# Performance work log

Hardware: AMD Instinct MI355X
Metric: run time of the kernel (lower is better)

The kernel has to match this reference:

```python
import jax, jax.numpy as jnp
import numpy as np

N = 65536
INPUT_DIM = 4
HIDDEN = 256
OUT_DIM = 64
NUM_FREQS = 10
NUM_LAYERS = 4  # -> 3 residual blocks
NUM_COMPOSE = 4
DIN_PE = INPUT_DIM + 2 * INPUT_DIM * NUM_FREQS  # 84


def setup_inputs() -> dict:
    key = jax.random.key(0)
    ks = jax.random.split(key, 10)
    x = jax.random.uniform(ks[0], (N, INPUT_DIM), jnp.float32, 0.1, 1.0)
    in_dim = jax.random.uniform(ks[1], (N,), jnp.float32, 0.5, 1.5)
    layer_id = jax.random.randint(ks[2], (N,), 0, NUM_COMPOSE, dtype=jnp.int32)
    s0 = 1.0 / np.sqrt(DIN_PE)
    sh = 1.0 / np.sqrt(HIDDEN)
    W0 = jax.random.normal(ks[3], (NUM_COMPOSE, DIN_PE, HIDDEN), jnp.float32) * s0
    b0 = jax.random.normal(ks[4], (NUM_COMPOSE, HIDDEN), jnp.float32) * s0
    Wh = jax.random.normal(ks[5], (NUM_COMPOSE, NUM_LAYERS - 1, HIDDEN, HIDDEN), jnp.float32) * sh
    bh = jax.random.normal(ks[6], (NUM_COMPOSE, NUM_LAYERS - 1, HIDDEN), jnp.float32) * sh
    scal = jax.random.normal(ks[7], (NUM_COMPOSE, NUM_LAYERS - 1), jnp.float32) * 0.5
    Wout = jax.random.normal(ks[8], (NUM_COMPOSE, HIDDEN, OUT_DIM), jnp.float32) * sh
    bout = jax.random.normal(ks[9], (NUM_COMPOSE, OUT_DIM), jnp.float32) * sh
    return {"x": x, "in_dim": in_dim, "layer_id": layer_id, "W0": W0, "b0": b0,
            "Wh": Wh, "bh": bh, "scal": scal, "Wout": Wout, "bout": bout}


def _positional_encoding(x):
    # x: [N, D]; out order matches torch: [x, (sin,cos) for each freq i, each dim j]
    freqs = (2.0 ** jnp.arange(NUM_FREQS, dtype=x.dtype)) * np.pi  # [F]
    ang = x[:, None, :] * freqs[None, :, None]                      # [N, F, D]
    sc = jnp.stack([jnp.sin(ang), jnp.cos(ang)], axis=-1)           # [N, F, D, 2]
    return jnp.concatenate([x, sc.reshape(x.shape[0], -1)], axis=1)  # [N, D+2FD]


def reference(x, in_dim, layer_id, W0, b0, Wh, bh, scal, Wout, bout):
    # x[:, :3] = x[:, :3] / x[:, 3:]
    x = jnp.concatenate([x[:, :3] / x[:, 3:4], x[:, 3:]], axis=1)
    xe = _positional_encoding(x)  # [N, 84]

    def one_model(W0c, b0c, Whc, bhc, sc, Woutc, boutc):
        h = jax.nn.relu(xe @ W0c + b0c)           # [N, H]
        for k in range(NUM_LAYERS - 1):
            h = sc[k] * jax.nn.relu(h @ Whc[k] + bhc[k]) + h
        return h @ Woutc + boutc                  # [N, Dout]

    outs = jax.vmap(one_model)(W0, b0, Wh, bh, scal, Wout, bout)  # [C, N, Dout]
    # dispatch/combine: select each row's expert output
    out = jnp.take_along_axis(outs.transpose(1, 0, 2),
                              layer_id[:, None, None], axis=1)[:, 0]  # [N, Dout]
    return out / in_dim[:, None]
```

## Files before the change

### kernel.cpp

```cpp
#include <hip/hip_runtime.h>
#include <hip/hip_bf16.h>
#include <math.h>

#define N_ROWS 65536
#define H 256
#define DOUT 64
#define NC 4
#define NLAYERS_HIDDEN 3
#define DIN_PE 84
#define KPE 96
#define XE_STRIDE 104
#define BM 64
#define FB_STRIDE 68

#define CHUNK 512
#define WT0_PER_E (3 * 16 * CHUNK)
#define WTH_PER_L (8 * 16 * CHUNK)
#define WTOUT_PER_E (8 * 4 * CHUNK)

using bf16 = __hip_bfloat16;
typedef __bf16 bf16x8 __attribute__((ext_vector_type(8)));
typedef float f32x4 __attribute__((ext_vector_type(4)));

__global__ void bucket_kernel(const int* __restrict__ layer_id,
                              int* __restrict__ gcnt, int* __restrict__ idx) {
  __shared__ int lcnt[NC];
  __shared__ int lbase[NC];
  const int tid = threadIdx.x;
  if (tid < NC) lcnt[tid] = 0;
  __syncthreads();
  const int i = blockIdx.x * blockDim.x + tid;
  const int e = layer_id[i];
  const int lp = atomicAdd(&lcnt[e], 1);
  __syncthreads();
  if (tid < NC) lbase[tid] = atomicAdd(&gcnt[tid], lcnt[tid]);
  __syncthreads();
  idx[e * N_ROWS + lbase[e] + lp] = i;
}

__global__ void prep_weights(const float* __restrict__ W0,
                             const float* __restrict__ Wh,
                             const float* __restrict__ Wout,
                             bf16* __restrict__ wt0, bf16* __restrict__ wth,
                             bf16* __restrict__ wtout) {
  const int n0 = NC * WT0_PER_E;
  const int nh = NC * 3 * WTH_PER_L;
  const int no = NC * WTOUT_PER_E;
  const int total = n0 + nh + no;
  for (int i = blockIdx.x * blockDim.x + threadIdx.x; i < total;
       i += gridDim.x * blockDim.x) {
    if (i < n0) {
      int c = i / WT0_PER_E; int r = i % WT0_PER_E;
      int kbi = r / (16 * CHUNK); int r2 = r % (16 * CHUNK);
      int nblk = r2 / CHUNK; int w = r2 % CHUNK;
      int lane = w / 8, j = w % 8;
      int n = nblk * 16 + (lane & 15);
      int k = kbi * 32 + (lane >> 4) * 8 + j;
      float v = (k < DIN_PE) ? W0[(c * DIN_PE + k) * H + n] : 0.f;
      wt0[i] = __float2bfloat16(v);
    } else if (i < n0 + nh) {
      int u = i - n0;
      int cl = u / WTH_PER_L; int r = u % WTH_PER_L;
      int kbi = r / (16 * CHUNK); int r2 = r % (16 * CHUNK);
      int nblk = r2 / CHUNK; int w = r2 % CHUNK;
      int lane = w / 8, j = w % 8;
      int n = nblk * 16 + (lane & 15);
      int k = kbi * 32 + (lane >> 4) * 8 + j;
      wth[u] = __float2bfloat16(Wh[(cl * H + k) * H + n]);
    } else {
      int u = i - n0 - nh;
      int c = u / WTOUT_PER_E; int r = u % WTOUT_PER_E;
      int kbi = r / (4 * CHUNK); int r2 = r % (4 * CHUNK);
      int nblk = r2 / CHUNK; int w = r2 % CHUNK;
      int lane = w / 8, j = w % 8;
      int n = nblk * 16 + (lane & 15);
      int k = kbi * 32 + (lane >> 4) * 8 + j;
      wtout[u] = __float2bfloat16(Wout[(c * H + k) * DOUT + n]);
    }
  }
}

__global__ __launch_bounds__(256, 3) void mlp_kernel(
    const float* __restrict__ x, const float* __restrict__ in_dim,
    const int* __restrict__ gcnt, const int* __restrict__ idx,
    const bf16* __restrict__ wt0, const float* __restrict__ b0,
    const bf16* __restrict__ wth, const float* __restrict__ bh,
    const float* __restrict__ scal, const bf16* __restrict__ wtout,
    const float* __restrict__ bout, float* __restrict__ out) {
  const int e = blockIdx.y;
  const int cnt = gcnt[e];
  const int base = blockIdx.x * BM;
  if (base >= cnt) return;

  __shared__ int ridx[BM];
  __shared__ float indim_s[BM];
  __shared__ __align__(16) char smem[BM * H * 2];
  bf16* xe = (bf16*)smem;
  bf16* hbuf = (bf16*)smem;
  float* fbuf = (float*)smem;

  const int tid = threadIdx.x;
  if (tid < BM) {
    int p = base + tid;
    int ri = (p < cnt) ? idx[e * N_ROWS + p] : -1;
    ridx[tid] = ri;
    indim_s[tid] = (ri >= 0) ? in_dim[ri] : 1.f;
  }
  __syncthreads();

  {
    const int r = tid >> 2, d = tid & 3;
    const int ri = ridx[r];
    float xd = 0.f, x3 = 1.f;
    if (ri >= 0) { xd = x[ri * 4 + d]; x3 = x[ri * 4 + 3]; }
    float v = (d < 3) ? (xd / x3) : x3;
    if (ri < 0) v = 0.f;
    bf16* row = xe + r * XE_STRIDE;
    row[d] = __float2bfloat16(v);
    float f = 3.14159265358979323846f;
#pragma unroll 1
    for (int q = 0; q < 10; ++q) {
      float sn, cs;
      __sincosf(v * f, &sn, &cs);
      row[4 + q * 8 + d * 2] = __float2bfloat16(sn);
      row[4 + q * 8 + d * 2 + 1] = __float2bfloat16(cs);
      f *= 2.f;
    }
#pragma unroll 1
    for (int c = DIN_PE + d; c < XE_STRIDE; c += 4) row[c] = __float2bfloat16(0.f);
  }
  __syncthreads();

  const int lane = tid & 63;
  const int wid = tid >> 6;
  const int l15 = lane & 15;
  const int lq = lane >> 4;
  const int wb = wid * 64;

  f32x4 acc[4][4];

  {
    const bf16* W = wt0 + (size_t)e * WT0_PER_E + lane * 8;
    const float* bias = b0 + e * H;
#pragma unroll
    for (int nt = 0; nt < 4; ++nt) {
      float b = bias[wb + nt * 16 + l15];
      f32x4 bv = {b, b, b, b};
#pragma unroll
      for (int mt = 0; mt < 4; ++mt) acc[mt][nt] = bv;
    }
#pragma unroll 1
    for (int kb = 0; kb < 3; ++kb) {
      bf16x8 a[4], bw[4];
#pragma unroll
      for (int nt = 0; nt < 4; ++nt)
        bw[nt] = *(const bf16x8*)(W + (kb * 16 + wid * 4 + nt) * CHUNK);
#pragma unroll
      for (int mt = 0; mt < 4; ++mt) {
        int row = mt * 16 + l15;
        a[mt] = *(const bf16x8*)(xe + row * XE_STRIDE + kb * 32 + lq * 8);
      }
#pragma unroll
      for (int mt = 0; mt < 4; ++mt)
#pragma unroll
        for (int nt = 0; nt < 4; ++nt)
          acc[mt][nt] = __builtin_amdgcn_mfma_f32_16x16x32_bf16(
              a[mt], bw[nt], acc[mt][nt], 0, 0, 0);
    }
    __syncthreads();
#pragma unroll
    for (int mt = 0; mt < 4; ++mt)
#pragma unroll
      for (int nt = 0; nt < 4; ++nt) {
        int col = wb + nt * 16 + l15;
#pragma unroll
        for (int j = 0; j < 4; ++j) {
          int row = mt * 16 + lq * 4 + j;
          float hv = fmaxf(acc[mt][nt][j], 0.f);
          int byte = (row * H + col) * 2;
          byte ^= ((row & 7) << 4);
          *(bf16*)((char*)hbuf + byte) = __float2bfloat16(hv);
        }
      }
  }
  __syncthreads();

#pragma unroll 1
  for (int l = 0; l < NLAYERS_HIDDEN; ++l) {
    const bf16* W = wth + (size_t)(e * 3 + l) * WTH_PER_L + lane * 8;
    const float* bias = bh + (e * 3 + l) * H;
    const float sc = scal[e * 3 + l];
#pragma unroll
    for (int nt = 0; nt < 4; ++nt) {
      float b = bias[wb + nt * 16 + l15];
      f32x4 bv = {b, b, b, b};
#pragma unroll
      for (int mt = 0; mt < 4; ++mt) acc[mt][nt] = bv;
    }
    bf16x8 bwc[4];
#pragma unroll
    for (int nt = 0; nt < 4; ++nt)
      bwc[nt] = *(const bf16x8*)(W + (wid * 4 + nt) * CHUNK);
#pragma unroll 1
    for (int kb = 0; kb < 8; ++kb) {
      bf16x8 bwn[4];
      int kn = (kb < 7) ? kb + 1 : kb;
#pragma unroll
      for (int nt = 0; nt < 4; ++nt)
        bwn[nt] = *(const bf16x8*)(W + (kn * 16 + wid * 4 + nt) * CHUNK);
      bf16x8 a[4];
#pragma unroll
      for (int mt = 0; mt < 4; ++mt) {
        int row = mt * 16 + l15;
        int byte = (row * H + kb * 32 + lq * 8) * 2;
        byte ^= ((row & 7) << 4);
        a[mt] = *(const bf16x8*)((const char*)hbuf + byte);
      }
#pragma unroll
      for (int mt = 0; mt < 4; ++mt)
#pragma unroll
        for (int nt = 0; nt < 4; ++nt)
          acc[mt][nt] = __builtin_amdgcn_mfma_f32_16x16x32_bf16(
              a[mt], bwc[nt], acc[mt][nt], 0, 0, 0);
#pragma unroll
      for (int nt = 0; nt < 4; ++nt) bwc[nt] = bwn[nt];
    }
    __syncthreads();
#pragma unroll
    for (int mt = 0; mt < 4; ++mt)
#pragma unroll
      for (int nt = 0; nt < 4; ++nt) {
        int col = wb + nt * 16 + l15;
#pragma unroll
        for (int j = 0; j < 4; ++j) {
          int row = mt * 16 + lq * 4 + j;
          int byte = (row * H + col) * 2;
          byte ^= ((row & 7) << 4);
          bf16* p = (bf16*)((char*)hbuf + byte);
          float hp = __bfloat162float(*p);
          float hv = sc * fmaxf(acc[mt][nt][j], 0.f) + hp;
          *p = __float2bfloat16(hv);
        }
      }
    __syncthreads();
  }

  {
    const bf16* W = wtout + (size_t)e * WTOUT_PER_E + lane * 8;
    const float* bias = bout + e * DOUT;
    f32x4 facc[4];
#pragma unroll
    for (int nt = 0; nt < 4; ++nt) {
      float b = bias[nt * 16 + l15];
      f32x4 bv = {b, b, b, b};
      facc[nt] = bv;
    }
    const int arow = wid * 16 + l15;
#pragma unroll 1
    for (int kb = 0; kb < 8; ++kb) {
      int byte = (arow * H + kb * 32 + lq * 8) * 2;
      byte ^= ((arow & 7) << 4);
      bf16x8 a = *(const bf16x8*)((const char*)hbuf + byte);
#pragma unroll
      for (int nt = 0; nt < 4; ++nt) {
        bf16x8 bw = *(const bf16x8*)(W + (kb * 4 + nt) * CHUNK);
        facc[nt] = __builtin_amdgcn_mfma_f32_16x16x32_bf16(a, bw, facc[nt], 0, 0, 0);
      }
    }
    __syncthreads();
#pragma unroll
    for (int nt = 0; nt < 4; ++nt) {
      int col = nt * 16 + l15;
#pragma unroll
      for (int j = 0; j < 4; ++j) {
        int row = wid * 16 + lq * 4 + j;
        fbuf[row * FB_STRIDE + col] = facc[nt][j];
      }
    }
  }
  __syncthreads();

#pragma unroll 1
  for (int p = 0; p < 4; ++p) {
    int item = p * 256 + tid;
    int row = item >> 4;
    int ch = item & 15;
    int ri = ridx[row];
    if (ri >= 0) {
      f32x4 v = *(const f32x4*)(fbuf + row * FB_STRIDE + ch * 4);
      float inv = indim_s[row];
      v[0] /= inv; v[1] /= inv; v[2] /= inv; v[3] /= inv;
      *(f32x4*)(out + (size_t)ri * DOUT + ch * 4) = v;
    }
  }
}

extern "C" void kernel_launch(void* const* d_in, const int* in_sizes, int n_in,
                              void* d_out, int out_size, void* d_ws,
                              size_t ws_size, hipStream_t stream) {
  const float* x = (const float*)d_in[0];
  const float* in_dim = (const float*)d_in[1];
  const int* layer_id = (const int*)d_in[2];
  const float* W0 = (const float*)d_in[3];
  const float* b0 = (const float*)d_in[4];
  const float* Wh = (const float*)d_in[5];
  const float* bh = (const float*)d_in[6];
  const float* scal = (const float*)d_in[7];
  const float* Wout = (const float*)d_in[8];
  const float* bout = (const float*)d_in[9];
  float* out = (float*)d_out;

  char* ws = (char*)d_ws;
  int* gcnt = (int*)ws;
  int* idx = (int*)(ws + 16);
  bf16* wt0 = (bf16*)(ws + 16 + (size_t)NC * N_ROWS * 4);
  bf16* wth = wt0 + NC * WT0_PER_E;
  bf16* wtout = wth + NC * 3 * WTH_PER_L;

  hipMemsetAsync(gcnt, 0, NC * sizeof(int), stream);
  bucket_kernel<<<N_ROWS / 256, 256, 0, stream>>>(layer_id, gcnt, idx);
  prep_weights<<<512, 256, 0, stream>>>(W0, Wh, Wout, wt0, wth, wtout);
  mlp_kernel<<<dim3(N_ROWS / BM, NC), 256, 0, stream>>>(
      x, in_dim, gcnt, idx, wt0, b0, wth, bh, scal, wtout, bout, out);
}
```

Before: 150.5 us.

## Flatten expert grid, double-buffer weight loads, raise occupancy bound

The 2D grid (blocks per expert × experts), most of whose blocks exited at once, becomes a 1D grid sized to the total row count. Each block finds its expert by prefix-summing the bucket counts. The hidden and output GEMM k-loops are unrolled by two with ping-pong register buffers, so each weight fragment load is issued a full k-step ahead. Launch bounds rise from 3 to 4 waves per SIMD, which limits registers and may cause spills, especially with the extra weight buffers.

```diff
diff --git a/kernel.cpp b/kernel.cpp
--- a/kernel.cpp
+++ b/kernel.cpp
@@ -80,17 +80,24 @@
   }
 }
 
-__global__ __launch_bounds__(256, 3) void mlp_kernel(
+__global__ __launch_bounds__(256, 4) void mlp_kernel(
     const float* __restrict__ x, const float* __restrict__ in_dim,
     const int* __restrict__ gcnt, const int* __restrict__ idx,
     const bf16* __restrict__ wt0, const float* __restrict__ b0,
     const bf16* __restrict__ wth, const float* __restrict__ bh,
     const float* __restrict__ scal, const bf16* __restrict__ wtout,
     const float* __restrict__ bout, float* __restrict__ out) {
-  const int e = blockIdx.y;
-  const int cnt = gcnt[e];
-  const int base = blockIdx.x * BM;
-  if (base >= cnt) return;
+  const int bid = blockIdx.x;
+  const int c0 = gcnt[0], c1 = gcnt[1], c2 = gcnt[2], c3 = gcnt[3];
+  const int n0 = (c0 + 63) >> 6, n1 = (c1 + 63) >> 6, n2 = (c2 + 63) >> 6,
+            n3 = (c3 + 63) >> 6;
+  int e, tb, cnt;
+  if (bid < n0) { e = 0; tb = bid; cnt = c0; }
+  else if (bid < n0 + n1) { e = 1; tb = bid - n0; cnt = c1; }
+  else if (bid < n0 + n1 + n2) { e = 2; tb = bid - n0 - n1; cnt = c2; }
+  else if (bid < n0 + n1 + n2 + n3) { e = 3; tb = bid - n0 - n1 - n2; cnt = c3; }
+  else return;
+  const int base = tb * BM;
 
   __shared__ int ridx[BM];
   __shared__ float indim_s[BM];
@@ -197,33 +204,51 @@
 #pragma unroll
       for (int mt = 0; mt < 4; ++mt) acc[mt][nt] = bv;
     }
-    bf16x8 bwc[4];
+    bf16x8 bw0[4], bw1[4];
 #pragma unroll
     for (int nt = 0; nt < 4; ++nt)
-      bwc[nt] = *(const bf16x8*)(W + (wid * 4 + nt) * CHUNK);
-#pragma unroll 1
-    for (int kb = 0; kb < 8; ++kb) {
-      bf16x8 bwn[4];
-      int kn = (kb < 7) ? kb + 1 : kb;
+      bw0[nt] = *(const bf16x8*)(W + (wid * 4 + nt) * CHUNK);
+#pragma unroll 1
+    for (int kb = 0; kb < 8; kb += 2) {
 #pragma unroll
       for (int nt = 0; nt < 4; ++nt)
-        bwn[nt] = *(const bf16x8*)(W + (kn * 16 + wid * 4 + nt) * CHUNK);
-      bf16x8 a[4];
-#pragma unroll
-      for (int mt = 0; mt < 4; ++mt) {
-        int row = mt * 16 + l15;
-        int byte = (row * H + kb * 32 + lq * 8) * 2;
-        byte ^= ((row & 7) << 4);
-        a[mt] = *(const bf16x8*)((const char*)hbuf + byte);
-      }
-#pragma unroll
-      for (int mt = 0; mt < 4; ++mt)
-#pragma unroll
-        for (int nt = 0; nt < 4; ++nt)
-          acc[mt][nt] = __builtin_amdgcn_mfma_f32_16x16x32_bf16(
-              a[mt], bwc[nt], acc[mt][nt], 0, 0, 0);
-#pragma unroll
-      for (int nt = 0; nt < 4; ++nt) bwc[nt] = bwn[nt];
+        bw1[nt] = *(const bf16x8*)(W + ((kb + 1) * 16 + wid * 4 + nt) * CHUNK);
+      {
+        bf16x8 a[4];
+#pragma unroll
+        for (int mt = 0; mt < 4; ++mt) {
+          int row = mt * 16 + l15;
+          int byte = (row * H + kb * 32 + lq * 8) * 2;
+          byte ^= ((row & 7) << 4);
+          a[mt] = *(const bf16x8*)((const char*)hbuf + byte);
+        }
+#pragma unroll
+        for (int mt = 0; mt < 4; ++mt)
+#pragma unroll
+          for (int nt = 0; nt < 4; ++nt)
+            acc[mt][nt] = __builtin_amdgcn_mfma_f32_16x16x32_bf16(
+                a[mt], bw0[nt], acc[mt][nt], 0, 0, 0);
+      }
+      {
+        int kn = (kb + 2) & 7;
+#pragma unroll
+        for (int nt = 0; nt < 4; ++nt)
+          bw0[nt] = *(const bf16x8*)(W + (kn * 16 + wid * 4 + nt) * CHUNK);
+        bf16x8 a[4];
+#pragma unroll
+        for (int mt = 0; mt < 4; ++mt) {
+          int row = mt * 16 + l15;
+          int byte = (row * H + (kb + 1) * 32 + lq * 8) * 2;
+          byte ^= ((row & 7) << 4);
+          a[mt] = *(const bf16x8*)((const char*)hbuf + byte);
+        }
+#pragma unroll
+        for (int mt = 0; mt < 4; ++mt)
+#pragma unroll
+          for (int nt = 0; nt < 4; ++nt)
+            acc[mt][nt] = __builtin_amdgcn_mfma_f32_16x16x32_bf16(
+                a[mt], bw1[nt], acc[mt][nt], 0, 0, 0);
+      }
     }
     __syncthreads();
 #pragma unroll
@@ -256,15 +281,34 @@
       facc[nt] = bv;
     }
     const int arow = wid * 16 + l15;
-#pragma unroll 1
-    for (int kb = 0; kb < 8; ++kb) {
-      int byte = (arow * H + kb * 32 + lq * 8) * 2;
-      byte ^= ((arow & 7) << 4);
-      bf16x8 a = *(const bf16x8*)((const char*)hbuf + byte);
-#pragma unroll
-      for (int nt = 0; nt < 4; ++nt) {
-        bf16x8 bw = *(const bf16x8*)(W + (kb * 4 + nt) * CHUNK);
-        facc[nt] = __builtin_amdgcn_mfma_f32_16x16x32_bf16(a, bw, facc[nt], 0, 0, 0);
+    bf16x8 bw0[4], bw1[4];
+#pragma unroll
+    for (int nt = 0; nt < 4; ++nt)
+      bw0[nt] = *(const bf16x8*)(W + nt * CHUNK);
+#pragma unroll 1
+    for (int kb = 0; kb < 8; kb += 2) {
+#pragma unroll
+      for (int nt = 0; nt < 4; ++nt)
+        bw1[nt] = *(const bf16x8*)(W + ((kb + 1) * 4 + nt) * CHUNK);
+      {
+        int byte = (arow * H + kb * 32 + lq * 8) * 2;
+        byte ^= ((arow & 7) << 4);
+        bf16x8 a = *(const bf16x8*)((const char*)hbuf + byte);
+#pragma unroll
+        for (int nt = 0; nt < 4; ++nt)
+          facc[nt] = __builtin_amdgcn_mfma_f32_16x16x32_bf16(a, bw0[nt], facc[nt], 0, 0, 0);
+      }
+      {
+        int kn = (kb + 2) & 7;
+#pragma unroll
+        for (int nt = 0; nt < 4; ++nt)
+          bw0[nt] = *(const bf16x8*)(W + (kn * 4 + nt) * CHUNK);
+        int byte = (arow * H + (kb + 1) * 32 + lq * 8) * 2;
+        byte ^= ((arow & 7) << 4);
+        bf16x8 a = *(const bf16x8*)((const char*)hbuf + byte);
+#pragma unroll
+        for (int nt = 0; nt < 4; ++nt)
+          facc[nt] = __builtin_amdgcn_mfma_f32_16x16x32_bf16(a, bw1[nt], facc[nt], 0, 0, 0);
       }
     }
     __syncthreads();
@@ -320,6 +364,6 @@
   hipMemsetAsync(gcnt, 0, NC * sizeof(int), stream);
   bucket_kernel<<<N_ROWS / 256, 256, 0, stream>>>(layer_id, gcnt, idx);
   prep_weights<<<512, 256, 0, stream>>>(W0, Wh, Wout, wt0, wth, wtout);
-  mlp_kernel<<<dim3(N_ROWS / BM, NC), 256, 0, stream>>>(
+  mlp_kernel<<<N_ROWS / BM + NC - 1, 256, 0, stream>>>(
       x, in_dim, gcnt, idx, wt0, b0, wth, bh, scal, wtout, bout, out);
 }
```

New measurement: 179.7 us. 19.4% more time.
